# Kernel tuning notes

Measured on AMD Instinct MI355X. Metric: run time of the kernel, lower is better.

Reference implementation:

```python
import jax, jax.numpy as jnp
import numpy as np

N_NODES = 100000
N_EDGES = 1600000
IN_DIM, HID, OUT = 128, 128, 64


def setup_inputs() -> dict:
    key = jax.random.key(0)
    ks = jax.random.split(key, 8)
    x = jax.random.normal(ks[0], (N_NODES, IN_DIM), dtype=jnp.float32)
    edge_index = jax.random.randint(ks[1], (2, N_EDGES), 0, N_NODES, dtype=jnp.int64)
    # Glorot-ish init for GCNConv linear weights (stored as [in, out]).
    W1 = jax.random.normal(ks[2], (IN_DIM, HID), dtype=jnp.float32) * (1.0 / np.sqrt(IN_DIM))
    b1 = jnp.zeros((HID,), dtype=jnp.float32)
    W2 = jax.random.normal(ks[3], (HID, HID), dtype=jnp.float32) * (1.0 / np.sqrt(HID))
    b2 = jnp.zeros((HID,), dtype=jnp.float32)
    W3 = jax.random.normal(ks[4], (HID, OUT), dtype=jnp.float32) * (1.0 / np.sqrt(HID))
    b3 = jnp.zeros((OUT,), dtype=jnp.float32)
    return {"x": x, "W1": W1, "b1": b1, "W2": W2, "b2": b2,
            "W3": W3, "b3": b3, "edge_index": edge_index}


def _gcn_norm(edge_index, num_nodes):
    # GCNConv default: add self loops, symmetric normalization D^{-1/2} A D^{-1/2}.
    loops = jnp.arange(num_nodes, dtype=edge_index.dtype)
    src = jnp.concatenate([edge_index[0], loops])
    dst = jnp.concatenate([edge_index[1], loops])
    deg = jax.ops.segment_sum(jnp.ones_like(dst, dtype=jnp.float32), dst,
                              num_segments=num_nodes)
    dinv = jnp.where(deg > 0, jax.lax.rsqrt(deg), 0.0)
    norm = dinv[src] * dinv[dst]  # [E + N]
    return src, dst, norm


def _gcn_conv(h, W, b, src, dst, norm, num_nodes):
    h = h @ W                                   # transform first (PyG GCNConv)
    msg = h[src] * norm[:, None]                # gather + scale
    agg = jax.ops.segment_sum(msg, dst, num_segments=num_nodes)  # scatter-add
    return agg + b


def _dropout(h, key, p=0.5):
    keep = jax.random.bernoulli(key, 1.0 - p, h.shape)
    return jnp.where(keep, h / (1.0 - p), 0.0)


def reference(x, W1, b1, W2, b2, W3, b3, edge_index):
    num_nodes = x.shape[0]
    src, dst, norm = _gcn_norm(edge_index, num_nodes)
    kd1, kd2 = jax.random.split(jax.random.key(42))
    h = jax.nn.relu(_gcn_conv(x, W1, b1, src, dst, norm, num_nodes))
    h = _dropout(h, kd1)
    h = jax.nn.relu(_gcn_conv(h, W2, b2, src, dst, norm, num_nodes))
    h = _dropout(h, kd2)
    return _gcn_conv(h, W3, b3, src, dst, norm, num_nodes)
```

## Files before the change

kernel.cpp:

```cpp
#include <hip/hip_runtime.h>
#include <stdint.h>

#define NN 100000
#define NE 1600000
#define NMASKW 400000
#define HIST_BLKS 6250
#define WSPL_BLKS 20

typedef float f4 __attribute__((ext_vector_type(4)));
typedef float f2 __attribute__((ext_vector_type(2)));
typedef unsigned short us4 __attribute__((ext_vector_type(4)));
typedef short s16x8 __attribute__((ext_vector_type(8)));

__device__ inline float bf2f(unsigned short u) {
  return __uint_as_float(((uint32_t)u) << 16);
}
__device__ inline unsigned short f2bf(float f) {
  uint32_t u = __float_as_uint(f);
  return (unsigned short)((u + 0x7fffu + ((u >> 16) & 1u)) >> 16);
}
__device__ inline float lo16(uint32_t q) { return __uint_as_float(q << 16); }
__device__ inline float hi16(uint32_t q) { return __uint_as_float(q & 0xffff0000u); }

__host__ __device__ inline void threefry2x32(uint32_t k0, uint32_t k1,
                                             uint32_t x0, uint32_t x1,
                                             uint32_t* y0, uint32_t* y1) {
  uint32_t ks[3] = {k0, k1, k0 ^ k1 ^ 0x1BD11BDAu};
  x0 += ks[0]; x1 += ks[1];
  const uint32_t R[2][4] = {{13u, 15u, 26u, 6u}, {17u, 29u, 16u, 24u}};
#pragma unroll
  for (int i = 0; i < 5; ++i) {
#pragma unroll
    for (int j = 0; j < 4; ++j) {
      uint32_t r = R[i & 1][j];
      x0 += x1;
      x1 = (x1 << r) | (x1 >> (32u - r));
      x1 ^= x0;
    }
    x0 += ks[(i + 1) % 3];
    x1 += ks[(i + 2) % 3] + (uint32_t)(i + 1);
  }
  *y0 = x0; *y1 = x1;
}

__device__ inline uint32_t tf_bits32(uint32_t k0, uint32_t k1, uint32_t idx) {
  uint32_t a, b;
  threefry2x32(k0, k1, 0u, idx, &a, &b);
  return a ^ b;
}

__global__ __launch_bounds__(256) void k_mask(uint32_t* __restrict__ m1,
                                              uint32_t* __restrict__ m2,
                                              uint32_t k10, uint32_t k11,
                                              uint32_t k20, uint32_t k21) {
  int t = blockIdx.x * 256 + threadIdx.x;
  if (t >= NMASKW) return;
  uint32_t base = (uint32_t)t * 32u;
  uint32_t w1 = 0, w2 = 0;
#pragma unroll 4
  for (int j = 0; j < 32; ++j) {
    w1 |= (tf_bits32(k10, k11, base + j) >> 31) << j;
    w2 |= (tf_bits32(k20, k21, base + j) >> 31) << j;
  }
  m1[t] = w1;
  m2[t] = w2;
}

__global__ void k_hist(const int* __restrict__ ei, uint32_t* __restrict__ cnt,
                       int* __restrict__ slot) {
  int e = blockIdx.x * 256 + threadIdx.x;
  if (e < NE) {
    int d = ei[NE + e];
    slot[e] = (int)atomicAdd(&cnt[d], 1u);
  }
}

__global__ __launch_bounds__(256) void k_scan1(const uint32_t* __restrict__ cnt,
                                               uint32_t* __restrict__ rp,
                                               uint32_t* __restrict__ bsum,
                                               float* __restrict__ dinv) {
  __shared__ uint32_t sh[256];
  int t = threadIdx.x;
  int base = blockIdx.x * 1024 + t * 4;
  uint32_t v[4];
  uint32_t s = 0;
#pragma unroll
  for (int i = 0; i < 4; ++i) {
    int idx = base + i;
    v[i] = (idx < NN) ? cnt[idx] : 0u;
    if (idx < NN) dinv[idx] = 1.0f / sqrtf((float)(v[i] + 1u));
    s += v[i];
  }
  sh[t] = s;
  __syncthreads();
  for (int off = 1; off < 256; off <<= 1) {
    uint32_t x = sh[t];
    if (t >= off) x += sh[t - off];
    __syncthreads();
    sh[t] = x;
    __syncthreads();
  }
  uint32_t run = (t > 0) ? sh[t - 1] : 0u;
  if (t == 255) bsum[blockIdx.x] = sh[255];
#pragma unroll
  for (int i = 0; i < 4; ++i) {
    int idx = base + i;
    if (idx < NN) rp[idx] = run;
    run += v[i];
  }
}

__global__ void k_scan2(uint32_t* bsum, int nb) {
  if (threadIdx.x == 0 && blockIdx.x == 0) {
    uint32_t s = 0;
    for (int i = 0; i < nb; ++i) { uint32_t x = bsum[i]; bsum[i] = s; s += x; }
  }
}

__global__ void k_scan3(uint32_t* rp, const uint32_t* __restrict__ bsum) {
  int i = blockIdx.x * 256 + threadIdx.x;
  if (i < NN) rp[i] += bsum[i >> 10];
  if (i == 0) rp[NN] = (uint32_t)NE;
}

__global__ __launch_bounds__(256) void k_scatwsplit(
    const int* __restrict__ ei, const uint32_t* __restrict__ rp,
    const int* __restrict__ slot, const float* __restrict__ dinv,
    uint2* __restrict__ e2,
    const float* __restrict__ W1, const float* __restrict__ W2,
    const float* __restrict__ W3,
    unsigned short* __restrict__ w1h, unsigned short* __restrict__ w1l,
    unsigned short* __restrict__ w2h, unsigned short* __restrict__ w2l,
    unsigned short* __restrict__ w3h, unsigned short* __restrict__ w3l) {
  int b = blockIdx.x;
  if (b < WSPL_BLKS) {
    int bb = b * 4 + (threadIdx.x >> 6);
    int lane = threadIdx.x & 63;
    const float* W; unsigned short *H, *L; int dout, j0;
    if (bb < 32)      { W = W1; H = w1h; L = w1l; dout = 128; j0 = bb; }
    else if (bb < 64) { W = W2; H = w2h; L = w2l; dout = 128; j0 = bb - 32; }
    else              { W = W3; H = w3h; L = w3l; dout = 64;  j0 = bb - 64; }
    int kk = j0 & 3;
    int ct = j0 >> 2;
    int kbase = kk * 32 + (lane >> 4) * 8;
    int col = ct * 16 + (lane & 15);
    us4 h0, h1, l0, l1;
#pragma unroll
    for (int j = 0; j < 4; ++j) {
      float v = W[(size_t)(kbase + j) * dout + col];
      h0[j] = f2bf(v);
      l0[j] = f2bf(v - bf2f(h0[j]));
      float v2 = W[(size_t)(kbase + 4 + j) * dout + col];
      h1[j] = f2bf(v2);
      l1[j] = f2bf(v2 - bf2f(h1[j]));
    }
    size_t o = ((size_t)j0 * 64 + lane) * 8;
    *(us4*)(H + o) = h0; *(us4*)(H + o + 4) = h1;
    *(us4*)(L + o) = l0; *(us4*)(L + o + 4) = l1;
  } else {
    int e = (b - WSPL_BLKS) * 256 + threadIdx.x;
    if (e < NE) {
      int s = ei[e];
      int d = ei[NE + e];
      float w = dinv[s] * dinv[d];
      uint2 rec;
      rec.x = (uint32_t)s;
      rec.y = __float_as_uint(w);
      e2[rp[d] + (uint32_t)slot[e]] = rec;
    }
  }
}

__global__ __launch_bounds__(256) void k_gemm1(
    const float* __restrict__ A, const unsigned short* __restrict__ Wh,
    const unsigned short* __restrict__ Wl, unsigned short* __restrict__ C) {
  constexpr int NT = 8;
  const int w = threadIdx.x >> 6;
  const int lane = threadIdx.x & 63;
  const int row0 = blockIdx.x * 64 + w * 16;
  int ar = row0 + (lane & 15);
  if (ar >= NN) ar = NN - 1;
  const int aoff = (lane >> 4) * 8;
  s16x8 afh[4], afl[4];
#pragma unroll
  for (int kk = 0; kk < 4; ++kk) {
    f4 v0 = *(const f4*)(A + (size_t)ar * 128 + kk * 32 + aoff);
    f4 v1 = *(const f4*)(A + (size_t)ar * 128 + kk * 32 + aoff + 4);
#pragma unroll
    for (int j = 0; j < 4; ++j) {
      unsigned short h = f2bf(v0[j]);
      afh[kk][j] = (short)h;
      afl[kk][j] = (short)f2bf(v0[j] - bf2f(h));
      unsigned short h2 = f2bf(v1[j]);
      afh[kk][j + 4] = (short)h2;
      afl[kk][j + 4] = (short)f2bf(v1[j] - bf2f(h2));
    }
  }
  f4 acc[NT];
#pragma unroll
  for (int t = 0; t < NT; ++t) acc[t] = (f4){0.f, 0.f, 0.f, 0.f};
#pragma unroll
  for (int ct = 0; ct < NT; ++ct) {
#pragma unroll
    for (int kk = 0; kk < 4; ++kk) {
      size_t bo = ((size_t)(ct * 4 + kk) * 64 + lane) * 8;
      s16x8 bh = *(const s16x8*)(Wh + bo);
      s16x8 bl = *(const s16x8*)(Wl + bo);
      acc[ct] = __builtin_amdgcn_mfma_f32_16x16x32_bf16(afh[kk], bh, acc[ct], 0, 0, 0);
      acc[ct] = __builtin_amdgcn_mfma_f32_16x16x32_bf16(afh[kk], bl, acc[ct], 0, 0, 0);
      acc[ct] = __builtin_amdgcn_mfma_f32_16x16x32_bf16(afl[kk], bh, acc[ct], 0, 0, 0);
    }
  }
  const int rbase = row0 + (lane >> 4) * 4;
  const int cbase = lane & 15;
#pragma unroll
  for (int ct = 0; ct < NT; ++ct) {
#pragma unroll
    for (int r = 0; r < 4; ++r) {
      int gr = rbase + r;
      if (gr < NN) C[(size_t)gr * 128 + ct * 16 + cbase] = f2bf(acc[ct][r]);
    }
  }
}

template <int DOUT>
__global__ __launch_bounds__(256) void k_gemm_mfma(
    const unsigned short* __restrict__ Ah, const unsigned short* __restrict__ Al,
    const unsigned short* __restrict__ Wh, const unsigned short* __restrict__ Wl,
    unsigned short* __restrict__ C) {
  constexpr int NT = DOUT / 16;
  const int w = threadIdx.x >> 6;
  const int lane = threadIdx.x & 63;
  const int row0 = blockIdx.x * 64 + w * 16;
  int ar = row0 + (lane & 15);
  if (ar >= NN) ar = NN - 1;
  const int aoff = (lane >> 4) * 8;
  s16x8 afh[4], afl[4];
#pragma unroll
  for (int kk = 0; kk < 4; ++kk) {
    afh[kk] = *(const s16x8*)(Ah + (size_t)ar * 128 + kk * 32 + aoff);
    afl[kk] = *(const s16x8*)(Al + (size_t)ar * 128 + kk * 32 + aoff);
  }
  f4 acc[NT];
#pragma unroll
  for (int t = 0; t < NT; ++t) acc[t] = (f4){0.f, 0.f, 0.f, 0.f};
#pragma unroll
  for (int ct = 0; ct < NT; ++ct) {
#pragma unroll
    for (int kk = 0; kk < 4; ++kk) {
      size_t bo = ((size_t)(ct * 4 + kk) * 64 + lane) * 8;
      s16x8 bh = *(const s16x8*)(Wh + bo);
      s16x8 bl = *(const s16x8*)(Wl + bo);
      acc[ct] = __builtin_amdgcn_mfma_f32_16x16x32_bf16(afh[kk], bh, acc[ct], 0, 0, 0);
      acc[ct] = __builtin_amdgcn_mfma_f32_16x16x32_bf16(afh[kk], bl, acc[ct], 0, 0, 0);
      acc[ct] = __builtin_amdgcn_mfma_f32_16x16x32_bf16(afl[kk], bh, acc[ct], 0, 0, 0);
    }
  }
  const int rbase = row0 + (lane >> 4) * 4;
  const int cbase = lane & 15;
#pragma unroll
  for (int ct = 0; ct < NT; ++ct) {
#pragma unroll
    for (int r = 0; r < 4; ++r) {
      int gr = rbase + r;
      if (gr < NN) C[(size_t)gr * DOUT + ct * 16 + cbase] = f2bf(acc[ct][r]);
    }
  }
}

__global__ __launch_bounds__(256) void k_agg_mid(
    const unsigned short* __restrict__ hb, const uint32_t* __restrict__ rp,
    const uint2* __restrict__ e2, const float* __restrict__ dinv,
    const float* __restrict__ bias, const uint32_t* __restrict__ mask,
    unsigned short* __restrict__ oh, unsigned short* __restrict__ ol) {
  int wid = __builtin_amdgcn_readfirstlane(blockIdx.x * 4 + (threadIdx.x >> 6));
  if (wid >= NN) return;
  const int lane = threadIdx.x & 63;
  const int q = lane >> 4;
  const int fl = lane & 15;
  const uint32_t beg = rp[wid], end = rp[wid + 1];
  const float dv = dinv[wid];
  const float sn = dv * dv;
  const char* hbase = (const char*)hb;
  f2 acc[4];
#pragma unroll
  for (int j = 0; j < 4; ++j) acc[j] = (f2){0.f, 0.f};

#define ACC4(g, wv)                                                        \
  {                                                                        \
    f2 wv2 = {wv, wv};                                                     \
    f2 h0 = {lo16(g.x), hi16(g.x)}; acc[0] += wv2 * h0;                    \
    f2 h1 = {lo16(g.y), hi16(g.y)}; acc[1] += wv2 * h1;                    \
    f2 h2 = {lo16(g.z), hi16(g.z)}; acc[2] += wv2 * h2;                    \
    f2 h3 = {lo16(g.w), hi16(g.w)}; acc[3] += wv2 * h3;                    \
  }

  uint32_t u = beg;
  for (; u + 16 <= end; u += 16) {
    uint2 r0 = e2[u + q];
    uint2 r1 = e2[u + 4 + q];
    uint2 r2 = e2[u + 8 + q];
    uint2 r3 = e2[u + 12 + q];
    uint4 g0 = *(const uint4*)(hbase + ((size_t)r0.x << 8) + fl * 16);
    uint4 g1 = *(const uint4*)(hbase + ((size_t)r1.x << 8) + fl * 16);
    uint4 g2 = *(const uint4*)(hbase + ((size_t)r2.x << 8) + fl * 16);
    uint4 g3 = *(const uint4*)(hbase + ((size_t)r3.x << 8) + fl * 16);
    float w0 = __uint_as_float(r0.y), w1 = __uint_as_float(r1.y);
    float w2 = __uint_as_float(r2.y), w3 = __uint_as_float(r3.y);
    ACC4(g0, w0); ACC4(g1, w1); ACC4(g2, w2); ACC4(g3, w3);
  }
  for (; u < end; u += 4) {
    uint32_t idx = u + (uint32_t)q;
    uint32_t cidx = idx < end ? idx : end - 1u;
    uint2 r = e2[cidx];
    float w = (idx < end) ? __uint_as_float(r.y) : 0.f;
    uint4 g = *(const uint4*)(hbase + ((size_t)r.x << 8) + fl * 16);
    ACC4(g, w);
  }
#undef ACC4

#pragma unroll
  for (int j = 0; j < 4; ++j) {
    acc[j][0] += __shfl_xor(acc[j][0], 16);
    acc[j][1] += __shfl_xor(acc[j][1], 16);
    acc[j][0] += __shfl_xor(acc[j][0], 32);
    acc[j][1] += __shfl_xor(acc[j][1], 32);
  }

  uint4 qs = *(const uint4*)(hbase + ((size_t)(uint32_t)wid << 8) + fl * 16);
  f2 snv = {sn, sn};
  f2 h0 = {lo16(qs.x), hi16(qs.x)};
  f2 h1 = {lo16(qs.y), hi16(qs.y)};
  f2 h2 = {lo16(qs.z), hi16(qs.z)};
  f2 h3 = {lo16(qs.w), hi16(qs.w)};
  acc[0] += snv * h0; acc[1] += snv * h1;
  acc[2] += snv * h2; acc[3] += snv * h3;
#pragma unroll
  for (int j = 0; j < 4; ++j) acc[j] += *(const f2*)(bias + fl * 8 + 2 * j);

  uint32_t mw = mask[(uint32_t)wid * 4u + (uint32_t)(fl >> 2)];
  uint32_t bb = (uint32_t)((fl & 3) * 8);
  uint32_t hw[4], lw[4];
#pragma unroll
  for (int j = 0; j < 4; ++j) {
    float a0 = fmaxf(acc[j][0], 0.f);
    float a1 = fmaxf(acc[j][1], 0.f);
    a0 = ((mw >> (bb + 2 * j)) & 1u) ? 0.f : a0 * 2.f;
    a1 = ((mw >> (bb + 2 * j + 1)) & 1u) ? 0.f : a1 * 2.f;
    unsigned short hh0 = f2bf(a0), hh1 = f2bf(a1);
    unsigned short g0 = f2bf(a0 - bf2f(hh0)), g1 = f2bf(a1 - bf2f(hh1));
    hw[j] = (uint32_t)hh0 | ((uint32_t)hh1 << 16);
    lw[j] = (uint32_t)g0 | ((uint32_t)g1 << 16);
  }
  if (q == 0) {
    uint4 v = {hw[0], hw[1], hw[2], hw[3]};
    *(uint4*)(oh + (size_t)(uint32_t)wid * 128 + fl * 8) = v;
  } else if (q == 1) {
    uint4 v = {lw[0], lw[1], lw[2], lw[3]};
    *(uint4*)(ol + (size_t)(uint32_t)wid * 128 + fl * 8) = v;
  }
}

__global__ __launch_bounds__(256) void k_agg_final(
    const unsigned short* __restrict__ hb, const uint32_t* __restrict__ rp,
    const uint2* __restrict__ e2, const float* __restrict__ dinv,
    const float* __restrict__ bias, float* __restrict__ out) {
  int wid = __builtin_amdgcn_readfirstlane(blockIdx.x * 4 + (threadIdx.x >> 6));
  if (wid >= NN) return;
  const int lane = threadIdx.x & 63;
  const int q = lane >> 4;
  const int fl = lane & 15;
  const uint32_t beg = rp[wid], end = rp[wid + 1];
  const float dv = dinv[wid];
  const float sn = dv * dv;
  const char* hbase = (const char*)hb;
  f2 acc[2];
  acc[0] = (f2){0.f, 0.f};
  acc[1] = (f2){0.f, 0.f};

#define ACC2(g, wv)                                                        \
  {                                                                        \
    f2 wv2 = {wv, wv};                                                     \
    f2 h0 = {lo16(g.x), hi16(g.x)}; acc[0] += wv2 * h0;                    \
    f2 h1 = {lo16(g.y), hi16(g.y)}; acc[1] += wv2 * h1;                    \
  }

  uint32_t u = beg;
  for (; u + 16 <= end; u += 16) {
    uint2 r0 = e2[u + q];
    uint2 r1 = e2[u + 4 + q];
    uint2 r2 = e2[u + 8 + q];
    uint2 r3 = e2[u + 12 + q];
    uint2 g0 = *(const uint2*)(hbase + ((size_t)r0.x << 7) + fl * 8);
    uint2 g1 = *(const uint2*)(hbase + ((size_t)r1.x << 7) + fl * 8);
    uint2 g2 = *(const uint2*)(hbase + ((size_t)r2.x << 7) + fl * 8);
    uint2 g3 = *(const uint2*)(hbase + ((size_t)r3.x << 7) + fl * 8);
    float w0 = __uint_as_float(r0.y), w1 = __uint_as_float(r1.y);
    float w2 = __uint_as_float(r2.y), w3 = __uint_as_float(r3.y);
    ACC2(g0, w0); ACC2(g1, w1); ACC2(g2, w2); ACC2(g3, w3);
  }
  for (; u < end; u += 4) {
    uint32_t idx = u + (uint32_t)q;
    uint32_t cidx = idx < end ? idx : end - 1u;
    uint2 r = e2[cidx];
    float w = (idx < end) ? __uint_as_float(r.y) : 0.f;
    uint2 g = *(const uint2*)(hbase + ((size_t)r.x << 7) + fl * 8);
    ACC2(g, w);
  }
#undef ACC2

#pragma unroll
  for (int j = 0; j < 2; ++j) {
    acc[j][0] += __shfl_xor(acc[j][0], 16);
    acc[j][1] += __shfl_xor(acc[j][1], 16);
    acc[j][0] += __shfl_xor(acc[j][0], 32);
    acc[j][1] += __shfl_xor(acc[j][1], 32);
  }

  uint2 qs = *(const uint2*)(hbase + ((size_t)(uint32_t)wid << 7) + fl * 8);
  f2 snv = {sn, sn};
  f2 h0 = {lo16(qs.x), hi16(qs.x)};
  f2 h1 = {lo16(qs.y), hi16(qs.y)};
  acc[0] += snv * h0;
  acc[1] += snv * h1;
  acc[0] += *(const f2*)(bias + fl * 4);
  acc[1] += *(const f2*)(bias + fl * 4 + 2);
  if (q == 0) {
    f4 v = {acc[0][0], acc[0][1], acc[1][0], acc[1][1]};
    *(f4*)(out + (size_t)(uint32_t)wid * 64 + fl * 4) = v;
  }
}

extern "C" void kernel_launch(void* const* d_in, const int* in_sizes, int n_in,
                              void* d_out, int out_size, void* d_ws, size_t ws_size,
                              hipStream_t stream) {
  (void)in_sizes; (void)n_in; (void)out_size; (void)ws_size;
  const float* x  = (const float*)d_in[0];
  const float* W1 = (const float*)d_in[1];
  const float* b1 = (const float*)d_in[2];
  const float* W2 = (const float*)d_in[3];
  const float* b2 = (const float*)d_in[4];
  const float* W3 = (const float*)d_in[5];
  const float* b3 = (const float*)d_in[6];
  const int* ei   = (const int*)d_in[7];
  float* out = (float*)d_out;

  char* p = (char*)d_ws;
  auto alloc = [&](size_t bytes) -> void* {
    void* r = (void*)p;
    p += (bytes + 255) & ~(size_t)255;
    return r;
  };
  uint32_t* cnt  = (uint32_t*)alloc((size_t)NN * 4);
  float*    dinv = (float*)alloc((size_t)NN * 4);
  uint32_t* rp   = (uint32_t*)alloc((size_t)(NN + 1) * 4);
  uint32_t* bsum = (uint32_t*)alloc(1024);
  int*      slot = (int*)alloc((size_t)NE * 4);
  uint2*    e2   = (uint2*)alloc((size_t)NE * 8);
  uint32_t* m1   = (uint32_t*)alloc((size_t)NMASKW * 4);
  uint32_t* m2   = (uint32_t*)alloc((size_t)NMASKW * 4);
  unsigned short* ah = (unsigned short*)alloc((size_t)NN * 128 * 2);
  unsigned short* al = (unsigned short*)alloc((size_t)NN * 128 * 2);
  unsigned short* hb = (unsigned short*)alloc((size_t)NN * 128 * 2);
  unsigned short* w1h = (unsigned short*)alloc(32 * 64 * 8 * 2);
  unsigned short* w1l = (unsigned short*)alloc(32 * 64 * 8 * 2);
  unsigned short* w2h = (unsigned short*)alloc(32 * 64 * 8 * 2);
  unsigned short* w2l = (unsigned short*)alloc(32 * 64 * 8 * 2);
  unsigned short* w3h = (unsigned short*)alloc(16 * 64 * 8 * 2);
  unsigned short* w3l = (unsigned short*)alloc(16 * 64 * 8 * 2);

  uint32_t kd1a, kd1b, kd2a, kd2b;
  threefry2x32(0u, 42u, 0u, 0u, &kd1a, &kd1b);
  threefry2x32(0u, 42u, 0u, 1u, &kd2a, &kd2b);

  const int gbN = (NN + 255) / 256;
  const int gbScan = (NN + 1023) / 1024;
  const int gbGemm = (NN + 63) / 64;
  const int gbAgg = (NN + 3) / 4;
  const int gbMask = (NMASKW + 255) / 256;

  hipMemsetAsync(cnt, 0, (size_t)NN * 4, stream);
  k_hist<<<HIST_BLKS, 256, 0, stream>>>(ei, cnt, slot);
  k_mask<<<gbMask, 256, 0, stream>>>(m1, m2, kd1a, kd1b, kd2a, kd2b);
  k_scan1<<<gbScan, 256, 0, stream>>>(cnt, rp, bsum, dinv);
  k_scan2<<<1, 64, 0, stream>>>(bsum, gbScan);
  k_scan3<<<gbN, 256, 0, stream>>>(rp, bsum);
  k_scatwsplit<<<WSPL_BLKS + HIST_BLKS, 256, 0, stream>>>(
      ei, rp, slot, dinv, e2, W1, W2, W3, w1h, w1l, w2h, w2l, w3h, w3l);

  k_gemm1<<<gbGemm, 256, 0, stream>>>(x, w1h, w1l, hb);
  k_agg_mid<<<gbAgg, 256, 0, stream>>>(hb, rp, e2, dinv, b1, m1, ah, al);
  k_gemm_mfma<128><<<gbGemm, 256, 0, stream>>>(ah, al, w2h, w2l, hb);
  k_agg_mid<<<gbAgg, 256, 0, stream>>>(hb, rp, e2, dinv, b2, m2, ah, al);
  k_gemm_mfma<64><<<gbGemm, 256, 0, stream>>>(ah, al, w3h, w3l, hb);
  k_agg_final<<<gbAgg, 256, 0, stream>>>(hb, rp, e2, dinv, b3, out);
}
```

Before: 431.7 us.

## Fuse histogram and dropout-mask kernels; process two row tiles per wave in GEMMs

Merges the edge-degree histogram and the threefry dropout-mask generation into one launch, interleaving four histogram blocks with one mask block so atomic-bound and compute-bound work overlap. Each GEMM wave now handles 32 rows in two 16-row groups, so every loaded weight fragment feeds twice as many MFMAs and the grid halves. This raises register pressure and may lower occupancy in the GEMM kernels.

```diff
diff --git a/kernel.cpp b/kernel.cpp
--- a/kernel.cpp
+++ b/kernel.cpp
@@ -49,29 +49,31 @@
   return a ^ b;
 }
 
-__global__ __launch_bounds__(256) void k_mask(uint32_t* __restrict__ m1,
-                                              uint32_t* __restrict__ m2,
-                                              uint32_t k10, uint32_t k11,
-                                              uint32_t k20, uint32_t k21) {
-  int t = blockIdx.x * 256 + threadIdx.x;
-  if (t >= NMASKW) return;
-  uint32_t base = (uint32_t)t * 32u;
-  uint32_t w1 = 0, w2 = 0;
+__global__ __launch_bounds__(256) void k_histmask(
+    const int* __restrict__ ei, uint32_t* __restrict__ cnt,
+    int* __restrict__ slot, uint32_t* __restrict__ m1, uint32_t* __restrict__ m2,
+    uint32_t k10, uint32_t k11, uint32_t k20, uint32_t k21) {
+  int b = blockIdx.x;
+  int q = b / 5, r = b % 5;
+  if (r < 4) {
+    int e = (q * 4 + r) * 256 + threadIdx.x;
+    if (e < NE) {
+      int d = ei[NE + e];
+      slot[e] = (int)atomicAdd(&cnt[d], 1u);
+    }
+  } else {
+    int t = q * 256 + threadIdx.x;
+    if (t < NMASKW) {
+      uint32_t base = (uint32_t)t * 32u;
+      uint32_t w1 = 0, w2 = 0;
 #pragma unroll 4
-  for (int j = 0; j < 32; ++j) {
-    w1 |= (tf_bits32(k10, k11, base + j) >> 31) << j;
-    w2 |= (tf_bits32(k20, k21, base + j) >> 31) << j;
-  }
-  m1[t] = w1;
-  m2[t] = w2;
-}
-
-__global__ void k_hist(const int* __restrict__ ei, uint32_t* __restrict__ cnt,
-                       int* __restrict__ slot) {
-  int e = blockIdx.x * 256 + threadIdx.x;
-  if (e < NE) {
-    int d = ei[NE + e];
-    slot[e] = (int)atomicAdd(&cnt[d], 1u);
+      for (int j = 0; j < 32; ++j) {
+        w1 |= (tf_bits32(k10, k11, base + j) >> 31) << j;
+        w2 |= (tf_bits32(k20, k21, base + j) >> 31) << j;
+      }
+      m1[t] = w1;
+      m2[t] = w2;
+    }
   }
 }
 
@@ -177,28 +179,33 @@
   constexpr int NT = 8;
   const int w = threadIdx.x >> 6;
   const int lane = threadIdx.x & 63;
-  const int row0 = blockIdx.x * 64 + w * 16;
-  int ar = row0 + (lane & 15);
-  if (ar >= NN) ar = NN - 1;
+  const int row0 = blockIdx.x * 128 + w * 32;
   const int aoff = (lane >> 4) * 8;
-  s16x8 afh[4], afl[4];
-#pragma unroll
-  for (int kk = 0; kk < 4; ++kk) {
-    f4 v0 = *(const f4*)(A + (size_t)ar * 128 + kk * 32 + aoff);
-    f4 v1 = *(const f4*)(A + (size_t)ar * 128 + kk * 32 + aoff + 4);
-#pragma unroll
-    for (int j = 0; j < 4; ++j) {
-      unsigned short h = f2bf(v0[j]);
-      afh[kk][j] = (short)h;
-      afl[kk][j] = (short)f2bf(v0[j] - bf2f(h));
-      unsigned short h2 = f2bf(v1[j]);
-      afh[kk][j + 4] = (short)h2;
-      afl[kk][j + 4] = (short)f2bf(v1[j] - bf2f(h2));
-    }
-  }
-  f4 acc[NT];
-#pragma unroll
-  for (int t = 0; t < NT; ++t) acc[t] = (f4){0.f, 0.f, 0.f, 0.f};
+  s16x8 afh[2][4], afl[2][4];
+#pragma unroll
+  for (int g = 0; g < 2; ++g) {
+    int ar = row0 + g * 16 + (lane & 15);
+    if (ar >= NN) ar = NN - 1;
+#pragma unroll
+    for (int kk = 0; kk < 4; ++kk) {
+      f4 v0 = *(const f4*)(A + (size_t)ar * 128 + kk * 32 + aoff);
+      f4 v1 = *(const f4*)(A + (size_t)ar * 128 + kk * 32 + aoff + 4);
+#pragma unroll
+      for (int j = 0; j < 4; ++j) {
+        unsigned short h = f2bf(v0[j]);
+        afh[g][kk][j] = (short)h;
+        afl[g][kk][j] = (short)f2bf(v0[j] - bf2f(h));
+        unsigned short h2 = f2bf(v1[j]);
+        afh[g][kk][j + 4] = (short)h2;
+        afl[g][kk][j + 4] = (short)f2bf(v1[j] - bf2f(h2));
+      }
+    }
+  }
+  f4 acc[2][NT];
+#pragma unroll
+  for (int g = 0; g < 2; ++g)
+#pragma unroll
+    for (int t = 0; t < NT; ++t) acc[g][t] = (f4){0.f, 0.f, 0.f, 0.f};
 #pragma unroll
   for (int ct = 0; ct < NT; ++ct) {
 #pragma unroll
@@ -206,19 +213,25 @@
       size_t bo = ((size_t)(ct * 4 + kk) * 64 + lane) * 8;
       s16x8 bh = *(const s16x8*)(Wh + bo);
       s16x8 bl = *(const s16x8*)(Wl + bo);
-      acc[ct] = __builtin_amdgcn_mfma_f32_16x16x32_bf16(afh[kk], bh, acc[ct], 0, 0, 0);
-      acc[ct] = __builtin_amdgcn_mfma_f32_16x16x32_bf16(afh[kk], bl, acc[ct], 0, 0, 0);
-      acc[ct] = __builtin_amdgcn_mfma_f32_16x16x32_bf16(afl[kk], bh, acc[ct], 0, 0, 0);
-    }
-  }
-  const int rbase = row0 + (lane >> 4) * 4;
+#pragma unroll
+      for (int g = 0; g < 2; ++g) {
+        acc[g][ct] = __builtin_amdgcn_mfma_f32_16x16x32_bf16(afh[g][kk], bh, acc[g][ct], 0, 0, 0);
+        acc[g][ct] = __builtin_amdgcn_mfma_f32_16x16x32_bf16(afh[g][kk], bl, acc[g][ct], 0, 0, 0);
+        acc[g][ct] = __builtin_amdgcn_mfma_f32_16x16x32_bf16(afl[g][kk], bh, acc[g][ct], 0, 0, 0);
+      }
+    }
+  }
   const int cbase = lane & 15;
 #pragma unroll
-  for (int ct = 0; ct < NT; ++ct) {
-#pragma unroll
-    for (int r = 0; r < 4; ++r) {
-      int gr = rbase + r;
-      if (gr < NN) C[(size_t)gr * 128 + ct * 16 + cbase] = f2bf(acc[ct][r]);
+  for (int g = 0; g < 2; ++g) {
+    const int rbase = row0 + g * 16 + (lane >> 4) * 4;
+#pragma unroll
+    for (int ct = 0; ct < NT; ++ct) {
+#pragma unroll
+      for (int r = 0; r < 4; ++r) {
+        int gr = rbase + r;
+        if (gr < NN) C[(size_t)gr * 128 + ct * 16 + cbase] = f2bf(acc[g][ct][r]);
+      }
     }
   }
 }
@@ -231,19 +244,24 @@
   constexpr int NT = DOUT / 16;
   const int w = threadIdx.x >> 6;
   const int lane = threadIdx.x & 63;
-  const int row0 = blockIdx.x * 64 + w * 16;
-  int ar = row0 + (lane & 15);
-  if (ar >= NN) ar = NN - 1;
+  const int row0 = blockIdx.x * 128 + w * 32;
   const int aoff = (lane >> 4) * 8;
-  s16x8 afh[4], afl[4];
-#pragma unroll
-  for (int kk = 0; kk < 4; ++kk) {
-    afh[kk] = *(const s16x8*)(Ah + (size_t)ar * 128 + kk * 32 + aoff);
-    afl[kk] = *(const s16x8*)(Al + (size_t)ar * 128 + kk * 32 + aoff);
-  }
-  f4 acc[NT];
-#pragma unroll
-  for (int t = 0; t < NT; ++t) acc[t] = (f4){0.f, 0.f, 0.f, 0.f};
+  s16x8 afh[2][4], afl[2][4];
+#pragma unroll
+  for (int g = 0; g < 2; ++g) {
+    int ar = row0 + g * 16 + (lane & 15);
+    if (ar >= NN) ar = NN - 1;
+#pragma unroll
+    for (int kk = 0; kk < 4; ++kk) {
+      afh[g][kk] = *(const s16x8*)(Ah + (size_t)ar * 128 + kk * 32 + aoff);
+      afl[g][kk] = *(const s16x8*)(Al + (size_t)ar * 128 + kk * 32 + aoff);
+    }
+  }
+  f4 acc[2][NT];
+#pragma unroll
+  for (int g = 0; g < 2; ++g)
+#pragma unroll
+    for (int t = 0; t < NT; ++t) acc[g][t] = (f4){0.f, 0.f, 0.f, 0.f};
 #pragma unroll
   for (int ct = 0; ct < NT; ++ct) {
 #pragma unroll
@@ -251,19 +269,25 @@
       size_t bo = ((size_t)(ct * 4 + kk) * 64 + lane) * 8;
       s16x8 bh = *(const s16x8*)(Wh + bo);
       s16x8 bl = *(const s16x8*)(Wl + bo);
-      acc[ct] = __builtin_amdgcn_mfma_f32_16x16x32_bf16(afh[kk], bh, acc[ct], 0, 0, 0);
-      acc[ct] = __builtin_amdgcn_mfma_f32_16x16x32_bf16(afh[kk], bl, acc[ct], 0, 0, 0);
-      acc[ct] = __builtin_amdgcn_mfma_f32_16x16x32_bf16(afl[kk], bh, acc[ct], 0, 0, 0);
-    }
-  }
-  const int rbase = row0 + (lane >> 4) * 4;
+#pragma unroll
+      for (int g = 0; g < 2; ++g) {
+        acc[g][ct] = __builtin_amdgcn_mfma_f32_16x16x32_bf16(afh[g][kk], bh, acc[g][ct], 0, 0, 0);
+        acc[g][ct] = __builtin_amdgcn_mfma_f32_16x16x32_bf16(afh[g][kk], bl, acc[g][ct], 0, 0, 0);
+        acc[g][ct] = __builtin_amdgcn_mfma_f32_16x16x32_bf16(afl[g][kk], bh, acc[g][ct], 0, 0, 0);
+      }
+    }
+  }
   const int cbase = lane & 15;
 #pragma unroll
-  for (int ct = 0; ct < NT; ++ct) {
-#pragma unroll
-    for (int r = 0; r < 4; ++r) {
-      int gr = rbase + r;
-      if (gr < NN) C[(size_t)gr * DOUT + ct * 16 + cbase] = f2bf(acc[ct][r]);
+  for (int g = 0; g < 2; ++g) {
+    const int rbase = row0 + g * 16 + (lane >> 4) * 4;
+#pragma unroll
+    for (int ct = 0; ct < NT; ++ct) {
+#pragma unroll
+      for (int r = 0; r < 4; ++r) {
+        int gr = rbase + r;
+        if (gr < NN) C[(size_t)gr * DOUT + ct * 16 + cbase] = f2bf(acc[g][ct][r]);
+      }
     }
   }
 }
@@ -475,13 +499,11 @@
 
   const int gbN = (NN + 255) / 256;
   const int gbScan = (NN + 1023) / 1024;
-  const int gbGemm = (NN + 63) / 64;
+  const int gbGemm = (NN + 127) / 128;
   const int gbAgg = (NN + 3) / 4;
-  const int gbMask = (NMASKW + 255) / 256;
 
   hipMemsetAsync(cnt, 0, (size_t)NN * 4, stream);
-  k_hist<<<HIST_BLKS, 256, 0, stream>>>(ei, cnt, slot);
-  k_mask<<<gbMask, 256, 0, stream>>>(m1, m2, kd1a, kd1b, kd2a, kd2b);
+  k_histmask<<<8000, 256, 0, stream>>>(ei, cnt, slot, m1, m2, kd1a, kd1b, kd2a, kd2b);
   k_scan1<<<gbScan, 256, 0, stream>>>(cnt, rp, bsum, dinv);
   k_scan2<<<1, 64, 0, stream>>>(bsum, gbScan);
   k_scan3<<<gbN, 256, 0, stream>>>(rp, bsum);
```

New measurement: 401.7 us. 1.07x faster.
